# Optimization experiments

Hardware: AMD Instinct MI355X
Metric: run time of the kernel (lower is better)

The kernel has to match this reference:

```python
import jax, jax.numpy as jnp
import numpy as np

N_NODES = 50000
N_EDGES = 1_600_000
IN_CH, HID_CH, OUT_CH, EDGE_DIM = 128, 128, 64, 16
NEG_SLOPE = 0.2


def _glorot(key, shape):
    fan = sum(shape) if len(shape) > 1 else shape[0] + 1
    lim = jnp.sqrt(6.0 / fan)
    return jax.random.uniform(key, shape, jnp.float32, -lim, lim)


def setup_inputs() -> dict:
    key = jax.random.key(0)
    ks = jax.random.split(key, 16)
    x = jax.random.normal(ks[0], (N_NODES, IN_CH), jnp.float32)
    edge_index = jax.random.randint(ks[1], (2, N_EDGES), 0, N_NODES, jnp.int32)
    flepe = jax.random.normal(ks[2], (N_EDGES, EDGE_DIM), jnp.float32)
    # layer 1 params (GATConv heads=1)
    W1 = _glorot(ks[3], (IN_CH, HID_CH))
    att_src1 = _glorot(ks[4], (HID_CH,))
    att_dst1 = _glorot(ks[5], (HID_CH,))
    We1 = _glorot(ks[6], (EDGE_DIM, HID_CH))
    att_edge1 = _glorot(ks[7], (HID_CH,))
    b1 = jnp.zeros((HID_CH,), jnp.float32)
    # layer 2 params
    W2 = _glorot(ks[8], (HID_CH, OUT_CH))
    att_src2 = _glorot(ks[9], (OUT_CH,))
    att_dst2 = _glorot(ks[10], (OUT_CH,))
    We2 = _glorot(ks[11], (EDGE_DIM, OUT_CH))
    att_edge2 = _glorot(ks[12], (OUT_CH,))
    b2 = jnp.zeros((OUT_CH,), jnp.float32)
    return {"x": x, "edge_index": edge_index, "flepe": flepe,
            "W1": W1, "att_src1": att_src1, "att_dst1": att_dst1,
            "We1": We1, "att_edge1": att_edge1, "b1": b1,
            "W2": W2, "att_src2": att_src2, "att_dst2": att_dst2,
            "We2": We2, "att_edge2": att_edge2, "b2": b2}


def gat_conv(x, src, dst, edge_attr, W, a_s, a_d, We, a_e, b, n_nodes):
    # PyG GATConv, heads=1, concat=True, negative_slope=0.2, edge_dim set.
    h = x @ W                                    # [N, C]
    alpha_src = h @ a_s                          # [N]
    alpha_dst = h @ a_d                          # [N]
    e = edge_attr @ We                           # [E, C]
    alpha_edge = e @ a_e                         # [E]
    alpha = alpha_src[src] + alpha_dst[dst] + alpha_edge
    alpha = jax.nn.leaky_relu(alpha, NEG_SLOPE)  # [E]
    # segment softmax over incoming edges per destination node
    amax = jax.ops.segment_max(alpha, dst, num_segments=n_nodes)
    amax = jnp.where(jnp.isfinite(amax), amax, 0.0)
    ex = jnp.exp(alpha - amax[dst])
    denom = jax.ops.segment_sum(ex, dst, num_segments=n_nodes)
    coef = ex / (denom[dst] + 1e-16)
    out = jax.ops.segment_sum(coef[:, None] * h[src], dst, num_segments=n_nodes)
    return out + b


def reference(x, edge_index, flepe,
              W1, att_src1, att_dst1, We1, att_edge1, b1,
              W2, att_src2, att_dst2, We2, att_edge2, b2):
    src, dst = edge_index[0], edge_index[1]
    n = x.shape[0]
    # dropout(p=0.5) is identity in eval mode
    h = gat_conv(x, src, dst, flepe, W1, att_src1, att_dst1, We1, att_edge1, b1, n)
    h = jax.nn.relu(h)
    out = gat_conv(h, src, dst, flepe, W2, att_src2, att_dst2, We2, att_edge2, b2, n)
    return out
```

## Files before the change

### kernel.cpp

```cpp
#include <hip/hip_runtime.h>
#include <hip/hip_bf16.h>

typedef unsigned int uint;
typedef __attribute__((ext_vector_type(8))) short bf16x8;
typedef __attribute__((ext_vector_type(4))) float f32x4;


__device__ inline float bf2f_lo(uint u) { return __uint_as_float((u & 0xffffu) << 16); }
__device__ inline float bf2f_hi(uint u) { return __uint_as_float(u & 0xffff0000u); }
__device__ inline uint f2bf_rne(float f) {
    uint x = __float_as_uint(f);
    return (x + 0x7fffu + ((x >> 16) & 1u)) >> 16;
}
__device__ inline uint pack_bf2(float a, float b) { return f2bf_rne(a) | (f2bf_rne(b) << 16); }

__global__ void k_prep(const float* __restrict__ W1, const float* __restrict__ W2,
                       uint4* __restrict__ S1, uint4* __restrict__ S2) {
    int t = blockIdx.x * 256 + threadIdx.x;
    if (t < 2048) {
        int f = t >> 6, l = t & 63;
        int kb = f >> 3, cb = f & 7;
        int k0 = kb * 32 + (l >> 4) * 8, c = cb * 16 + (l & 15);
        uint u[4];
#pragma unroll
        for (int m = 0; m < 4; ++m)
            u[m] = pack_bf2(W1[(k0 + 2 * m) * 128 + c], W1[(k0 + 2 * m + 1) * 128 + c]);
        S1[t] = make_uint4(u[0], u[1], u[2], u[3]);
    } else if (t < 3072) {
        int tt = t - 2048;
        int f = tt >> 6, l = tt & 63;
        int kb = f >> 2, cb = f & 3;
        int k0 = kb * 32 + (l >> 4) * 8, c = cb * 16 + (l & 15);
        uint u[4];
#pragma unroll
        for (int m = 0; m < 4; ++m)
            u[m] = pack_bf2(W2[(k0 + 2 * m) * 64 + c], W2[(k0 + 2 * m + 1) * 64 + c]);
        S2[tt] = make_uint4(u[0], u[1], u[2], u[3]);
    }
}

__global__ void k_deg(const int* __restrict__ dst, int* __restrict__ deg, int E,
                      const float* __restrict__ We1, const float* __restrict__ ae1w,
                      const float* __restrict__ We2, const float* __restrict__ ae2w,
                      float* __restrict__ p1, float* __restrict__ p2) {
    if (blockIdx.x == 0) {
        int t = threadIdx.x;
        if (t < 16) {
            float s = 0.f;
            for (int c = 0; c < 128; ++c) s += We1[t * 128 + c] * ae1w[c];
            p1[t] = s;
        } else if (t < 32) {
            int d = t - 16;
            float s = 0.f;
            for (int c = 0; c < 64; ++c) s += We2[d * 64 + c] * ae2w[c];
            p2[d] = s;
        }
    }
    int e = blockIdx.x * blockDim.x + threadIdx.x;
    if (e < E) atomicAdd(&deg[dst[e]], 1);
}

__global__ __launch_bounds__(1024) void k_scanA(const int* __restrict__ deg,
                                                int* __restrict__ excl,
                                                int* __restrict__ bsum, int N) {
    __shared__ int s[1024];
    int tid = threadIdx.x;
    int gid = blockIdx.x * 1024 + tid;
    int v = (gid < N) ? deg[gid] : 0;
    s[tid] = v;
    __syncthreads();
    for (int off = 1; off < 1024; off <<= 1) {
        int t = (tid >= off) ? s[tid - off] : 0;
        __syncthreads();
        s[tid] += t;
        __syncthreads();
    }
    if (gid < N) excl[gid] = s[tid] - v;
    if (tid == 1023) bsum[blockIdx.x] = s[1023];
}

__global__ void k_scanB(const int* __restrict__ bsum, int* __restrict__ bsumx, int nb,
                        int* __restrict__ rowstart, int N, int E) {
    int t = threadIdx.x;
    int v = (t < nb) ? bsum[t] : 0;
    int x = v;
    for (int o = 1; o < 64; o <<= 1) {
        int y = __shfl_up(x, o);
        if (t >= o) x += y;
    }
    if (t < nb) bsumx[t] = x - v;
    if (t == 0) rowstart[N] = E;
}

__global__ __launch_bounds__(1024) void k_scanC(const int* __restrict__ excl,
                                                const int* __restrict__ bsumx,
                                                int* __restrict__ rowstart,
                                                int* __restrict__ cursor, int N) {
    int gid = blockIdx.x * 1024 + threadIdx.x;
    if (gid < N) {
        int v = excl[gid] + bsumx[blockIdx.x];
        rowstart[gid] = v;
        cursor[gid] = v;
    }
}

__global__ void k_scat(const int* __restrict__ src, const int* __restrict__ dst,
                       const float* __restrict__ fe,
                       const float* __restrict__ p1, const float* __restrict__ p2,
                       int* __restrict__ cursor, float4* __restrict__ rec, int E) {
    float q1[16], q2[16];
#pragma unroll
    for (int i = 0; i < 16; ++i) { q1[i] = p1[i]; q2[i] = p2[i]; }
    int e = blockIdx.x * blockDim.x + threadIdx.x;
    if (e >= E) return;
    int s = src[e], d = dst[e];
    const float4* f = reinterpret_cast<const float4*>(fe) + (size_t)e * 4;
    float a1 = 0.f, a2 = 0.f;
#pragma unroll
    for (int j = 0; j < 4; ++j) {
        float4 v = f[j];
        a1 += v.x * q1[4 * j] + v.y * q1[4 * j + 1] + v.z * q1[4 * j + 2] + v.w * q1[4 * j + 3];
        a2 += v.x * q2[4 * j] + v.y * q2[4 * j + 1] + v.z * q2[4 * j + 2] + v.w * q2[4 * j + 3];
    }
    int pos = atomicAdd(&cursor[d], 1);
    rec[pos] = make_float4(__int_as_float(s), a1, a2, 0.f);
}

template <int COUT, bool BF16IN>
__global__ __launch_bounds__(256) void k_gemm_mfma(
    const void* __restrict__ Xv, const uint4* __restrict__ Wswz,
    const float* __restrict__ avs, const float* __restrict__ avd,
    uint* __restrict__ Hb, float* __restrict__ asrc, float* __restrict__ adst,
    int ntiles) {
    constexpr int NCB = COUT / 16;
    constexpr int NFRAG = NCB * 4;
    __shared__ uint4 WB[NFRAG * 64];
    for (int i = threadIdx.x; i < NFRAG * 64; i += 256) WB[i] = Wswz[i];
    __syncthreads();
    const int wv = threadIdx.x >> 6, l = threadIdx.x & 63;
    const int lrow = l & 15, lkq = l >> 4;

    float vs[NCB], vd[NCB];
#pragma unroll
    for (int cb = 0; cb < NCB; ++cb) {
        vs[cb] = avs[cb * 16 + lrow];
        vd[cb] = avd[cb * 16 + lrow];
    }
    union U16 { uint4 q; bf16x8 v; };

    for (int t = blockIdx.x * 4 + wv; t < ntiles; t += gridDim.x * 4) {
        const int rowb = t * 16;
        const int r0 = rowb + lrow;
        bf16x8 a[4];
        if constexpr (BF16IN) {
            const uint4* xr4 = reinterpret_cast<const uint4*>(Xv) + (size_t)r0 * 16;
#pragma unroll
            for (int kb = 0; kb < 4; ++kb) {
                U16 cv; cv.q = xr4[kb * 4 + lkq];
                a[kb] = cv.v;
            }
        } else {
            const float* xr = reinterpret_cast<const float*>(Xv) + (size_t)r0 * 128 + lkq * 8;
#pragma unroll
            for (int kb = 0; kb < 4; ++kb) {
                float4 f0 = *reinterpret_cast<const float4*>(xr + kb * 32);
                float4 f1 = *reinterpret_cast<const float4*>(xr + kb * 32 + 4);
                U16 cv;
                cv.q = make_uint4(pack_bf2(f0.x, f0.y), pack_bf2(f0.z, f0.w),
                                  pack_bf2(f1.x, f1.y), pack_bf2(f1.z, f1.w));
                a[kb] = cv.v;
            }
        }
        f32x4 acc[NCB];
#pragma unroll
        for (int cb = 0; cb < NCB; ++cb) acc[cb] = (f32x4){0.f, 0.f, 0.f, 0.f};
#pragma unroll
        for (int cb = 0; cb < NCB; ++cb) {
#pragma unroll
            for (int kb = 0; kb < 4; ++kb) {
                U16 bu;
                bu.q = WB[(kb * NCB + cb) * 64 + l];
                acc[cb] = __builtin_amdgcn_mfma_f32_16x16x32_bf16(a[kb], bu.v, acc[cb], 0, 0, 0);
            }
        }
        float ps[4] = {0.f, 0.f, 0.f, 0.f}, pd[4] = {0.f, 0.f, 0.f, 0.f};
#pragma unroll
        for (int cb = 0; cb < NCB; ++cb) {
#pragma unroll
            for (int r = 0; r < 4; ++r) {
                float v = acc[cb][r];
                ps[r] += v * vs[cb];
                pd[r] += v * vd[cb];
                float pv = __shfl_xor(v, 1);
                if (!(l & 1))
                    Hb[(size_t)(rowb + lkq * 4 + r) * (COUT / 2) + cb * 8 + (lrow >> 1)] =
                        pack_bf2(v, pv);
            }
        }
#pragma unroll
        for (int o = 1; o < 16; o <<= 1) {
#pragma unroll
            for (int r = 0; r < 4; ++r) {
                ps[r] += __shfl_xor(ps[r], o);
                pd[r] += __shfl_xor(pd[r], o);
            }
        }
        if (lrow == 0) {
            int rb = rowb + lkq * 4;
#pragma unroll
            for (int r = 0; r < 4; ++r) { asrc[rb + r] = ps[r]; adst[rb + r] = pd[r]; }
        }
    }
}

__global__ __launch_bounds__(256) void k_aggr1(
    const int* __restrict__ rowstart, const float4* __restrict__ rec,
    const float* __restrict__ asrc, const float* __restrict__ adst,
    const uint* __restrict__ Hb, const float* __restrict__ bias,
    uint* __restrict__ out, int N) {
    __shared__ uint2 swl[4][64];
    const int wv = threadIdx.x >> 6, lane = threadIdx.x & 63;
    int n = blockIdx.x * 4 + wv;
    if (n >= N) return;
    n = __builtin_amdgcn_readfirstlane(n);
    int s = rowstart[n], e = rowstart[n + 1];
    float ad = adst[n];
    float a0 = 0.f, a1 = 0.f, ws = 0.f;
    for (int base = s; base < e; base += 64) {
        int cnt = e - base; if (cnt > 64) cnt = 64;
        float w = 0.f; int sn = 0;
        if (lane < cnt) {
            float4 rc = rec[base + lane];
            sn = __float_as_int(rc.x);
            float al = asrc[sn] + ad + rc.y;
            al = al > 0.f ? al : 0.2f * al;
            w = __expf(al);
        }
        float wsum = w;
        for (int o = 32; o; o >>= 1) wsum += __shfl_xor(wsum, o);
        ws += wsum;
        swl[wv][lane] = make_uint2((uint)sn, __float_as_uint(w));
        int cnt4 = (cnt + 3) & ~3;
        for (int j = 0; j < cnt4; j += 4) {
            uint2 t0 = swl[wv][j], t1 = swl[wv][j + 1], t2 = swl[wv][j + 2], t3 = swl[wv][j + 3];
            uint h0 = Hb[(size_t)t0.x * 64 + lane];
            uint h1 = Hb[(size_t)t1.x * 64 + lane];
            uint h2 = Hb[(size_t)t2.x * 64 + lane];
            uint h3 = Hb[(size_t)t3.x * 64 + lane];
            float w0 = __uint_as_float(t0.y), w1 = __uint_as_float(t1.y);
            float w2 = __uint_as_float(t2.y), w3 = __uint_as_float(t3.y);
            a0 = fmaf(w0, bf2f_lo(h0), a0); a1 = fmaf(w0, bf2f_hi(h0), a1);
            a0 = fmaf(w1, bf2f_lo(h1), a0); a1 = fmaf(w1, bf2f_hi(h1), a1);
            a0 = fmaf(w2, bf2f_lo(h2), a0); a1 = fmaf(w2, bf2f_hi(h2), a1);
            a0 = fmaf(w3, bf2f_lo(h3), a0); a1 = fmaf(w3, bf2f_hi(h3), a1);
        }
    }
    float inv = 1.0f / (ws + 1e-16f);
    float2 b2 = reinterpret_cast<const float2*>(bias)[lane];
    float o0 = fmaxf(fmaf(a0, inv, b2.x), 0.f);
    float o1 = fmaxf(fmaf(a1, inv, b2.y), 0.f);
    out[(size_t)n * 64 + lane] = pack_bf2(o0, o1);
}

__global__ __launch_bounds__(256) void k_aggr2(
    const int* __restrict__ rowstart, const float4* __restrict__ rec,
    const float* __restrict__ asrc, const float* __restrict__ adst,
    const uint* __restrict__ Hb, const float* __restrict__ bias,
    float* __restrict__ out, int N) {
    __shared__ uint2 swl[4][64];
    const int wv = threadIdx.x >> 6, lane = threadIdx.x & 63;
    const int half = lane >> 5, hl = lane & 31;
    int n = blockIdx.x * 4 + wv;
    if (n >= N) return;
    n = __builtin_amdgcn_readfirstlane(n);
    int s = rowstart[n], e = rowstart[n + 1];
    float ad = adst[n];
    float a0 = 0.f, a1 = 0.f, ws = 0.f;
    for (int base = s; base < e; base += 64) {
        int cnt = e - base; if (cnt > 64) cnt = 64;
        float w = 0.f; int sn = 0;
        if (lane < cnt) {
            float4 rc = rec[base + lane];
            sn = __float_as_int(rc.x);
            float al = asrc[sn] + ad + rc.z;
            al = al > 0.f ? al : 0.2f * al;
            w = __expf(al);
        }
        float wsum = w;
        for (int o = 32; o; o >>= 1) wsum += __shfl_xor(wsum, o);
        ws += wsum;
        swl[wv][lane] = make_uint2((uint)sn, __float_as_uint(w));
        int cnt4 = (cnt + 3) & ~3;
        for (int j = 0; j < cnt4; j += 4) {
            uint2 t0 = swl[wv][j + half];
            uint2 t1 = swl[wv][j + 2 + half];
            uint h0 = Hb[(size_t)t0.x * 32 + hl];
            uint h1 = Hb[(size_t)t1.x * 32 + hl];
            float w0 = __uint_as_float(t0.y), w1 = __uint_as_float(t1.y);
            a0 = fmaf(w0, bf2f_lo(h0), a0); a1 = fmaf(w0, bf2f_hi(h0), a1);
            a0 = fmaf(w1, bf2f_lo(h1), a0); a1 = fmaf(w1, bf2f_hi(h1), a1);
        }
    }
    a0 += __shfl_xor(a0, 32);
    a1 += __shfl_xor(a1, 32);
    if (half == 0) {
        float inv = 1.0f / (ws + 1e-16f);
        float2 b2 = reinterpret_cast<const float2*>(bias)[hl];
        reinterpret_cast<float2*>(out)[(size_t)n * 32 + hl] =
            make_float2(fmaf(a0, inv, b2.x), fmaf(a1, inv, b2.y));
    }
}

extern "C" void kernel_launch(void* const* d_in, const int* in_sizes, int n_in,
                              void* d_out, int out_size, void* d_ws, size_t ws_size,
                              hipStream_t stream) {
    const float* x    = (const float*)d_in[0];
    const int*   ei   = (const int*)d_in[1];
    const float* fe   = (const float*)d_in[2];
    const float* W1   = (const float*)d_in[3];
    const float* as1  = (const float*)d_in[4];
    const float* ad1  = (const float*)d_in[5];
    const float* We1  = (const float*)d_in[6];
    const float* ae1w = (const float*)d_in[7];
    const float* b1   = (const float*)d_in[8];
    const float* W2   = (const float*)d_in[9];
    const float* as2  = (const float*)d_in[10];
    const float* ad2  = (const float*)d_in[11];
    const float* We2  = (const float*)d_in[12];
    const float* ae2w = (const float*)d_in[13];
    const float* b2   = (const float*)d_in[14];
    float* out = (float*)d_out;

    const int N = in_sizes[0] / 128;
    const int E = in_sizes[1] / 2;
    const int* src = ei;
    const int* dst = ei + E;

    char* ws = (char*)d_ws;
    size_t off = 0;
    auto alloc = [&](size_t bytes) -> void* {
        void* p = ws + off;
        off = (off + bytes + 255) & ~(size_t)255;
        return p;
    };
    float*  p1       = (float*)alloc(64);
    float*  p2       = (float*)alloc(64);
    uint4*  S1       = (uint4*)alloc(2048 * 16);
    uint4*  S2       = (uint4*)alloc(1024 * 16);
    float4* rec      = (float4*)alloc((size_t)E * 16);
    uint*   x2       = (uint*)alloc((size_t)N * 64 * 4);
    uint*   H1       = (uint*)alloc((size_t)N * 64 * 4);
    uint*   H2       = (uint*)alloc((size_t)N * 32 * 4);
    float*  asrc     = (float*)alloc((size_t)N * 4);
    float*  adst     = (float*)alloc((size_t)N * 4);
    int*    deg      = (int*)alloc((size_t)N * 4);
    int*    excl     = (int*)alloc((size_t)N * 4);
    int*    rowstart = (int*)alloc((size_t)(N + 1) * 4);
    int*    cursor   = (int*)alloc((size_t)N * 4);
    int*    bsum     = (int*)alloc(256);
    int*    bsumx    = (int*)alloc(256);

    const int nb = (N + 1023) / 1024;
    const int ntiles = (N + 15) / 16;

    hipMemsetAsync(deg, 0, (size_t)N * 4, stream);
    k_prep<<<12, 256, 0, stream>>>(W1, W2, S1, S2);
    k_deg<<<(E + 255) / 256, 256, 0, stream>>>(dst, deg, E, We1, ae1w, We2, ae2w, p1, p2);
    k_scanA<<<nb, 1024, 0, stream>>>(deg, excl, bsum, N);
    k_scanB<<<1, 64, 0, stream>>>(bsum, bsumx, nb, rowstart, N, E);
    k_scanC<<<nb, 1024, 0, stream>>>(excl, bsumx, rowstart, cursor, N);
    k_scat<<<(E + 255) / 256, 256, 0, stream>>>(src, dst, fe, p1, p2, cursor, rec, E);

    k_gemm_mfma<128, false><<<512, 256, 0, stream>>>(x, S1, as1, ad1, H1, asrc, adst, ntiles);
    k_aggr1<<<(N + 3) / 4, 256, 0, stream>>>(rowstart, rec, asrc, adst, H1, b1, x2, N);

    k_gemm_mfma<64, true><<<512, 256, 0, stream>>>(x2, S2, as2, ad2, H2, asrc, adst, ntiles);
    k_aggr2<<<(N + 3) / 4, 256, 0, stream>>>(rowstart, rec, asrc, adst, H2, b2, out, N);
}
```

Measured before the change: 438.1 us.

## Vectorize aggregation gathers to 16-byte loads with edge-parallel lane groups

Both aggregation kernels now have each lane load a 16-byte chunk of a neighbor's bf16 feature row, so several edges are processed in parallel across lane groups instead of one 4-byte word per lane per edge. Per-lane partial sums are reduced with cross-lane shuffles at the end, and the output is written as wide vector stores. The scatter kernel issues its cursor atomic earlier and writes edge records with nontemporal stores. The intent is fewer, wider gather instructions and better latency hiding. The cost is extra registers for eight accumulators, a shuffle reduction per node, and wasted lanes when a node has few edges.

```diff
diff --git a/kernel.cpp b/kernel.cpp
--- a/kernel.cpp
+++ b/kernel.cpp
@@ -107,13 +107,14 @@
 __global__ void k_scat(const int* __restrict__ src, const int* __restrict__ dst,
                        const float* __restrict__ fe,
                        const float* __restrict__ p1, const float* __restrict__ p2,
-                       int* __restrict__ cursor, float4* __restrict__ rec, int E) {
+                       int* __restrict__ cursor, f32x4* __restrict__ rec, int E) {
     float q1[16], q2[16];
 #pragma unroll
     for (int i = 0; i < 16; ++i) { q1[i] = p1[i]; q2[i] = p2[i]; }
     int e = blockIdx.x * blockDim.x + threadIdx.x;
     if (e >= E) return;
     int s = src[e], d = dst[e];
+    int pos = atomicAdd(&cursor[d], 1);
     const float4* f = reinterpret_cast<const float4*>(fe) + (size_t)e * 4;
     float a1 = 0.f, a2 = 0.f;
 #pragma unroll
@@ -122,8 +123,8 @@
         a1 += v.x * q1[4 * j] + v.y * q1[4 * j + 1] + v.z * q1[4 * j + 2] + v.w * q1[4 * j + 3];
         a2 += v.x * q2[4 * j] + v.y * q2[4 * j + 1] + v.z * q2[4 * j + 2] + v.w * q2[4 * j + 3];
     }
-    int pos = atomicAdd(&cursor[d], 1);
-    rec[pos] = make_float4(__int_as_float(s), a1, a2, 0.f);
+    f32x4 r = {__int_as_float(s), a1, a2, 0.f};
+    __builtin_nontemporal_store(r, rec + pos);
 }
 
 template <int COUT, bool BF16IN>
@@ -216,16 +217,20 @@
 __global__ __launch_bounds__(256) void k_aggr1(
     const int* __restrict__ rowstart, const float4* __restrict__ rec,
     const float* __restrict__ asrc, const float* __restrict__ adst,
-    const uint* __restrict__ Hb, const float* __restrict__ bias,
-    uint* __restrict__ out, int N) {
+    const uint4* __restrict__ H4, const float* __restrict__ bias,
+    uint4* __restrict__ out4, int N) {
     __shared__ uint2 swl[4][64];
     const int wv = threadIdx.x >> 6, lane = threadIdx.x & 63;
+    const int eg = lane >> 4, ch = lane & 15;
     int n = blockIdx.x * 4 + wv;
     if (n >= N) return;
     n = __builtin_amdgcn_readfirstlane(n);
     int s = rowstart[n], e = rowstart[n + 1];
     float ad = adst[n];
-    float a0 = 0.f, a1 = 0.f, ws = 0.f;
+    float acc[8];
+#pragma unroll
+    for (int k = 0; k < 8; ++k) acc[k] = 0.f;
+    float ws = 0.f;
     for (int base = s; base < e; base += 64) {
         int cnt = e - base; if (cnt > 64) cnt = 64;
         float w = 0.f; int sn = 0;
@@ -242,40 +247,53 @@
         swl[wv][lane] = make_uint2((uint)sn, __float_as_uint(w));
         int cnt4 = (cnt + 3) & ~3;
         for (int j = 0; j < cnt4; j += 4) {
-            uint2 t0 = swl[wv][j], t1 = swl[wv][j + 1], t2 = swl[wv][j + 2], t3 = swl[wv][j + 3];
-            uint h0 = Hb[(size_t)t0.x * 64 + lane];
-            uint h1 = Hb[(size_t)t1.x * 64 + lane];
-            uint h2 = Hb[(size_t)t2.x * 64 + lane];
-            uint h3 = Hb[(size_t)t3.x * 64 + lane];
-            float w0 = __uint_as_float(t0.y), w1 = __uint_as_float(t1.y);
-            float w2 = __uint_as_float(t2.y), w3 = __uint_as_float(t3.y);
-            a0 = fmaf(w0, bf2f_lo(h0), a0); a1 = fmaf(w0, bf2f_hi(h0), a1);
-            a0 = fmaf(w1, bf2f_lo(h1), a0); a1 = fmaf(w1, bf2f_hi(h1), a1);
-            a0 = fmaf(w2, bf2f_lo(h2), a0); a1 = fmaf(w2, bf2f_hi(h2), a1);
-            a0 = fmaf(w3, bf2f_lo(h3), a0); a1 = fmaf(w3, bf2f_hi(h3), a1);
-        }
-    }
-    float inv = 1.0f / (ws + 1e-16f);
-    float2 b2 = reinterpret_cast<const float2*>(bias)[lane];
-    float o0 = fmaxf(fmaf(a0, inv, b2.x), 0.f);
-    float o1 = fmaxf(fmaf(a1, inv, b2.y), 0.f);
-    out[(size_t)n * 64 + lane] = pack_bf2(o0, o1);
+            uint2 t = swl[wv][j + eg];
+            float w0 = __uint_as_float(t.y);
+            uint4 h = H4[(size_t)t.x * 16 + ch];
+            acc[0] = fmaf(w0, bf2f_lo(h.x), acc[0]); acc[1] = fmaf(w0, bf2f_hi(h.x), acc[1]);
+            acc[2] = fmaf(w0, bf2f_lo(h.y), acc[2]); acc[3] = fmaf(w0, bf2f_hi(h.y), acc[3]);
+            acc[4] = fmaf(w0, bf2f_lo(h.z), acc[4]); acc[5] = fmaf(w0, bf2f_hi(h.z), acc[5]);
+            acc[6] = fmaf(w0, bf2f_lo(h.w), acc[6]); acc[7] = fmaf(w0, bf2f_hi(h.w), acc[7]);
+        }
+    }
+#pragma unroll
+    for (int o = 16; o <= 32; o <<= 1)
+#pragma unroll
+        for (int k = 0; k < 8; ++k) acc[k] += __shfl_xor(acc[k], o);
+    if (eg == 0) {
+        float inv = 1.0f / (ws + 1e-16f);
+        float4 b0 = reinterpret_cast<const float4*>(bias)[ch * 2];
+        float4 b1 = reinterpret_cast<const float4*>(bias)[ch * 2 + 1];
+        float o0 = fmaxf(fmaf(acc[0], inv, b0.x), 0.f);
+        float o1 = fmaxf(fmaf(acc[1], inv, b0.y), 0.f);
+        float o2 = fmaxf(fmaf(acc[2], inv, b0.z), 0.f);
+        float o3 = fmaxf(fmaf(acc[3], inv, b0.w), 0.f);
+        float o4 = fmaxf(fmaf(acc[4], inv, b1.x), 0.f);
+        float o5 = fmaxf(fmaf(acc[5], inv, b1.y), 0.f);
+        float o6 = fmaxf(fmaf(acc[6], inv, b1.z), 0.f);
+        float o7 = fmaxf(fmaf(acc[7], inv, b1.w), 0.f);
+        out4[(size_t)n * 16 + ch] = make_uint4(pack_bf2(o0, o1), pack_bf2(o2, o3),
+                                               pack_bf2(o4, o5), pack_bf2(o6, o7));
+    }
 }
 
 __global__ __launch_bounds__(256) void k_aggr2(
     const int* __restrict__ rowstart, const float4* __restrict__ rec,
     const float* __restrict__ asrc, const float* __restrict__ adst,
-    const uint* __restrict__ Hb, const float* __restrict__ bias,
+    const uint4* __restrict__ H4, const float* __restrict__ bias,
     float* __restrict__ out, int N) {
     __shared__ uint2 swl[4][64];
     const int wv = threadIdx.x >> 6, lane = threadIdx.x & 63;
-    const int half = lane >> 5, hl = lane & 31;
+    const int eg = lane >> 3, ch = lane & 7;
     int n = blockIdx.x * 4 + wv;
     if (n >= N) return;
     n = __builtin_amdgcn_readfirstlane(n);
     int s = rowstart[n], e = rowstart[n + 1];
     float ad = adst[n];
-    float a0 = 0.f, a1 = 0.f, ws = 0.f;
+    float acc[8];
+#pragma unroll
+    for (int k = 0; k < 8; ++k) acc[k] = 0.f;
+    float ws = 0.f;
     for (int base = s; base < e; base += 64) {
         int cnt = e - base; if (cnt > 64) cnt = 64;
         float w = 0.f; int sn = 0;
@@ -290,24 +308,32 @@
         for (int o = 32; o; o >>= 1) wsum += __shfl_xor(wsum, o);
         ws += wsum;
         swl[wv][lane] = make_uint2((uint)sn, __float_as_uint(w));
-        int cnt4 = (cnt + 3) & ~3;
-        for (int j = 0; j < cnt4; j += 4) {
-            uint2 t0 = swl[wv][j + half];
-            uint2 t1 = swl[wv][j + 2 + half];
-            uint h0 = Hb[(size_t)t0.x * 32 + hl];
-            uint h1 = Hb[(size_t)t1.x * 32 + hl];
-            float w0 = __uint_as_float(t0.y), w1 = __uint_as_float(t1.y);
-            a0 = fmaf(w0, bf2f_lo(h0), a0); a1 = fmaf(w0, bf2f_hi(h0), a1);
-            a0 = fmaf(w1, bf2f_lo(h1), a0); a1 = fmaf(w1, bf2f_hi(h1), a1);
-        }
-    }
-    a0 += __shfl_xor(a0, 32);
-    a1 += __shfl_xor(a1, 32);
-    if (half == 0) {
+        int cnt8 = (cnt + 7) & ~7;
+        for (int j = 0; j < cnt8; j += 8) {
+            uint2 t = swl[wv][j + eg];
+            float w0 = __uint_as_float(t.y);
+            uint4 h = H4[(size_t)t.x * 8 + ch];
+            acc[0] = fmaf(w0, bf2f_lo(h.x), acc[0]); acc[1] = fmaf(w0, bf2f_hi(h.x), acc[1]);
+            acc[2] = fmaf(w0, bf2f_lo(h.y), acc[2]); acc[3] = fmaf(w0, bf2f_hi(h.y), acc[3]);
+            acc[4] = fmaf(w0, bf2f_lo(h.z), acc[4]); acc[5] = fmaf(w0, bf2f_hi(h.z), acc[5]);
+            acc[6] = fmaf(w0, bf2f_lo(h.w), acc[6]); acc[7] = fmaf(w0, bf2f_hi(h.w), acc[7]);
+        }
+    }
+#pragma unroll
+    for (int o = 8; o <= 32; o <<= 1)
+#pragma unroll
+        for (int k = 0; k < 8; ++k) acc[k] += __shfl_xor(acc[k], o);
+    if (eg == 0) {
         float inv = 1.0f / (ws + 1e-16f);
-        float2 b2 = reinterpret_cast<const float2*>(bias)[hl];
-        reinterpret_cast<float2*>(out)[(size_t)n * 32 + hl] =
-            make_float2(fmaf(a0, inv, b2.x), fmaf(a1, inv, b2.y));
+        float4 b0 = reinterpret_cast<const float4*>(bias)[ch * 2];
+        float4 b1 = reinterpret_cast<const float4*>(bias)[ch * 2 + 1];
+        float4 o0 = make_float4(fmaf(acc[0], inv, b0.x), fmaf(acc[1], inv, b0.y),
+                                fmaf(acc[2], inv, b0.z), fmaf(acc[3], inv, b0.w));
+        float4 o1 = make_float4(fmaf(acc[4], inv, b1.x), fmaf(acc[5], inv, b1.y),
+                                fmaf(acc[6], inv, b1.z), fmaf(acc[7], inv, b1.w));
+        float4* op = reinterpret_cast<float4*>(out + (size_t)n * 64 + ch * 8);
+        op[0] = o0;
+        op[1] = o1;
     }
 }
 
@@ -369,11 +395,14 @@
     k_scanA<<<nb, 1024, 0, stream>>>(deg, excl, bsum, N);
     k_scanB<<<1, 64, 0, stream>>>(bsum, bsumx, nb, rowstart, N, E);
     k_scanC<<<nb, 1024, 0, stream>>>(excl, bsumx, rowstart, cursor, N);
-    k_scat<<<(E + 255) / 256, 256, 0, stream>>>(src, dst, fe, p1, p2, cursor, rec, E);
+    k_scat<<<(E + 255) / 256, 256, 0, stream>>>(src, dst, fe, p1, p2, cursor,
+                                                (f32x4*)rec, E);
 
     k_gemm_mfma<128, false><<<512, 256, 0, stream>>>(x, S1, as1, ad1, H1, asrc, adst, ntiles);
-    k_aggr1<<<(N + 3) / 4, 256, 0, stream>>>(rowstart, rec, asrc, adst, H1, b1, x2, N);
+    k_aggr1<<<(N + 3) / 4, 256, 0, stream>>>(rowstart, rec, asrc, adst,
+                                             (const uint4*)H1, b1, (uint4*)x2, N);
 
     k_gemm_mfma<64, true><<<512, 256, 0, stream>>>(x2, S2, as2, ad2, H2, asrc, adst, ntiles);
-    k_aggr2<<<(N + 3) / 4, 256, 0, stream>>>(rowstart, rec, asrc, adst, H2, b2, out, N);
-}
+    k_aggr2<<<(N + 3) / 4, 256, 0, stream>>>(rowstart, rec, asrc, adst,
+                                             (const uint4*)H2, b2, out, N);
+}
```

New measurement: 462.5 us. 5.6% more time.
